# Performance work log

Hardware: AMD Instinct MI355X
Metric: run time of the kernel (lower is better)

## Reference

```python
import jax, jax.numpy as jnp
import numpy as np

N, E, S, K, NB = 16384, 262144, 10, 64, 8
R_MAX, P_CUT, AVG_NEIGH = 5.0, 5, 16.0
L_OF_LM = np.array([0, 1, 1, 1, 2, 2, 2, 2, 2])  # l value of each of the 9 lm components
L_SLICES = [(0, 1), (1, 4), (4, 9)]               # lm ranges for l = 0,1,2
MLP_H = 16


def _sph(u):
    # real spherical harmonics up to l=2, e3nn 'component' normalization (sum_m Y_lm^2 = 2l+1)
    x, y, z = u[..., 0], u[..., 1], u[..., 2]
    s3, s15, s5 = np.float32(np.sqrt(3.0)), np.float32(np.sqrt(15.0)), np.float32(np.sqrt(5.0))
    return jnp.stack([
        jnp.ones_like(x),
        s3 * x, s3 * y, s3 * z,
        s15 * x * y, s15 * y * z, (s5 / 2) * (3 * z * z - 1), s15 * x * z, (s15 / 2) * (x * x - y * y),
    ], axis=-1)


def _radial(r):
    # Bessel radial basis with smooth polynomial cutoff envelope (p = P_CUT)
    u = r / R_MAX
    r_safe = jnp.where(r > 1e-9, r, 1.0)
    n = jnp.arange(1, NB + 1, dtype=r.dtype)
    bess = np.float32(np.sqrt(2.0 / R_MAX)) * jnp.sin(n * jnp.pi * u[:, None]) / r_safe[:, None]
    p = float(P_CUT)
    env = 1.0 - (p + 1) * (p + 2) / 2 * u**P_CUT + p * (p + 2) * u**(P_CUT + 1) - p * (p + 1) / 2 * u**(P_CUT + 2)
    env = jnp.where(u < 1.0, env, 0.0)
    return bess * env[:, None]  # [E, NB]


def setup_inputs() -> dict:
    key = jax.random.key(0)
    ks = jax.random.split(key, 16)
    positions = jax.random.uniform(ks[0], (N, 3), jnp.float32) * 4.0  # box so many edges fall inside r_max
    species = jax.random.randint(ks[1], (N,), 0, S)
    senders = jax.random.randint(ks[2], (E,), 0, N)
    receivers = jax.random.randint(ks[3], (E,), 0, N)
    shifts = jnp.zeros((E, 3), jnp.float32)
    W_embed = jax.random.normal(ks[4], (S, K), jnp.float32)
    W_rad = jax.random.normal(ks[5], (2, 3, NB, K), jnp.float32) * 0.3
    W_mix = jax.random.normal(ks[6], (2, 3, K, K), jnp.float32) / np.sqrt(K)
    W_prod = jax.random.normal(ks[7], (2, 3, 3, K), jnp.float32) * 0.1
    W_sc = jax.random.normal(ks[8], (2, S, 3, K, K), jnp.float32) / np.sqrt(K)
    W_ro0 = jax.random.normal(ks[9], (K,), jnp.float32) / np.sqrt(K)
    W_m1 = jax.random.normal(ks[10], (K, MLP_H), jnp.float32) / np.sqrt(K)
    b_m1 = jnp.zeros((MLP_H,), jnp.float32)
    W_m2 = jax.random.normal(ks[11], (MLP_H,), jnp.float32) / np.sqrt(MLP_H)
    return dict(positions=positions, shifts=shifts, species=species, senders=senders,
                receivers=receivers, W_embed=W_embed, W_rad=W_rad, W_mix=W_mix,
                W_prod=W_prod, W_sc=W_sc, W_ro0=W_ro0, W_m1=W_m1, b_m1=b_m1, W_m2=W_m2)


def reference(positions, shifts, species, senders, receivers, W_embed, W_rad, W_mix,
              W_prod, W_sc, W_ro0, W_m1, b_m1, W_m2):
    lm = jnp.asarray(L_OF_LM)
    onehot = jax.nn.one_hot(species, S, dtype=positions.dtype)
    # node embedding: scalars only -> feats [N, 9(lm), K]
    feats = jnp.zeros((N, 9, K), positions.dtype).at[:, 0, :].set(onehot @ W_embed)

    # edge geometry
    vec = positions[receivers] - positions[senders] + shifts           # [E, 3]
    r = jnp.linalg.norm(vec, axis=-1)                                  # [E]
    u_hat = vec / jnp.where(r > 1e-9, r, 1.0)[:, None]
    Y = _sph(u_hat)                                                     # [E, 9]
    rad = _radial(r)                                                    # [E, NB]

    energies = []
    for i in range(2):
        # interaction: radial-weighted SH messages from sender scalars, scatter-sum to receivers
        hs = feats[:, 0, :][senders]                                    # [E, K]
        Rl = jnp.einsum('eb,lbk->elk', rad, W_rad[i])[:, lm, :]         # [E, 9, K]
        msg = hs[:, None, :] * Y[:, :, None] * Rl                       # [E, 9, K]
        A = jax.ops.segment_sum(msg, receivers, num_segments=N) / AVG_NEIGH
        A = jnp.einsum('nmk,mkj->nmj', A, W_mix[i][lm])                 # per-l channel mixing

        # correlation-3 equivariant product basis (symmetric-contraction style)
        A0 = A[:, 0, :]
        inv = jnp.sum(A * A, axis=1)                                    # rotation-invariant [N, K]
        w1, w2, w3 = (W_prod[i, j][lm] for j in range(3))               # each [9, K]
        B = A * (w1[None] + w2[None] * A0[:, None, :] + w3[None] * inv[:, None, :])

        # species-dependent self-connection (linear of feats x node_attrs), per-l weights
        sc = jnp.concatenate([
            jnp.einsum('nmk,ns,skj->nmj', feats[:, st:en], onehot, W_sc[i, :, l])
            for l, (st, en) in enumerate(L_SLICES)], axis=1)
        feats = B + sc

        if i == 0:
            energies.append(feats[:, 0, :] @ W_ro0)                     # linear readout
        else:
            feats = feats.at[:, 1:, :].set(0.0)                         # last layer keeps 0e only
            energies.append(jax.nn.silu(feats[:, 0, :] @ W_m1 + b_m1) @ W_m2)

    return jnp.stack(energies, axis=1)  # [N, num_interactions]
```

## Files before the change

kernel.cpp:

```cpp
#include <hip/hip_runtime.h>

#define NN 16384
#define NE 262144
#define NSPEC 10
#define KC 64
#define MLPH 16
#define SEG 128
#define EPSG 2048

typedef float v2f __attribute__((ext_vector_type(2)));

__device__ __forceinline__ float wave_reduce(float v) {
#pragma unroll
    for (int off = 32; off > 0; off >>= 1) v += __shfl_down(v, off, 64);
    return v;
}

__device__ __forceinline__ float f4c(const float4& v, int j) {
    const float* p = &v.x;
    return p[j];
}

__global__ void __launch_bounds__(1024) k_pre(
    const float* __restrict__ W_embed,
    const int* __restrict__ species,
    const int* __restrict__ receivers,
    int* __restrict__ eslot,
    unsigned short* __restrict__ cnt16,
    float4* __restrict__ h04) {
    __shared__ int cntL[NN];
    int t = threadIdx.x;
#pragma unroll
    for (int i = 0; i < 16; ++i) cntL[t + 1024 * i] = 0;
    __syncthreads();
    int ebase = blockIdx.x * EPSG;
#pragma unroll
    for (int j = 0; j < EPSG / 1024; ++j) {
        int e = ebase + j * 1024 + t;
        int r = receivers[e];
        eslot[e] = atomicAdd(&cntL[r], 1);
    }
    int gt = blockIdx.x * 1024 + t;
#pragma unroll
    for (int q = 0; q < 2; ++q) {
        int idx = gt * 2 + q;
        int n = idx >> 4, w = idx & 15;
        h04[idx] = reinterpret_cast<const float4*>(W_embed + species[n] * KC)[w];
    }
    __syncthreads();
    unsigned short* o = cnt16 + (size_t)blockIdx.x * NN;
#pragma unroll
    for (int i = 0; i < 16; ++i)
        o[t + 1024 * i] = (unsigned short)cntL[t + 1024 * i];
}

__global__ void __launch_bounds__(256) k_colscan(
    const unsigned short* __restrict__ cnt16,
    int* __restrict__ seg_base,
    int* __restrict__ count) {
    int lane = threadIdx.x & 63;
    int r = blockIdx.x * 4 + (threadIdx.x >> 6);
    int c0 = cnt16[(size_t)(2 * lane) * NN + r];
    int c1 = cnt16[(size_t)(2 * lane + 1) * NN + r];
    int s = c0 + c1;
    int inc = s;
#pragma unroll
    for (int off = 1; off < 64; off <<= 1) {
        int v = __shfl_up(inc, off, 64);
        if (lane >= off) inc += v;
    }
    int exc = inc - s;
    seg_base[(size_t)(2 * lane) * NN + r] = exc;
    seg_base[(size_t)(2 * lane + 1) * NN + r] = exc + c0;
    if (lane == 63) count[r] = inc;
}

__global__ void __launch_bounds__(1024) k_scan(
    const int* __restrict__ count, int* __restrict__ row_start,
    const int* __restrict__ species, int* __restrict__ nslot,
    int* __restrict__ sp_start) {
    __shared__ int lds[1024];
    __shared__ int itercnt[256 * NSPEC];
    __shared__ int spt[NSPEC];
    int t = threadIdx.x;
    int lane = t & 63;
    int w = t >> 6;
#pragma unroll
    for (int j = 0; j < 16; ++j) {
        int n = w * 1024 + j * 64 + lane;
        int sp = species[n];
#pragma unroll
        for (int s = 0; s < NSPEC; ++s) {
            unsigned long long mask = __ballot(sp == s);
            if (lane == 0) itercnt[(w * 16 + j) * NSPEC + s] = (int)__popcll(mask);
        }
    }
    int base = t * 16;
    int local[16];
    int ssum = 0;
#pragma unroll
    for (int b = 0; b < 16; ++b) { local[b] = count[base + b]; ssum += local[b]; }
    lds[t] = ssum;
    __syncthreads();
    for (int off = 1; off < 1024; off <<= 1) {
        int v = (t >= off) ? lds[t - off] : 0;
        __syncthreads();
        lds[t] += v;
        __syncthreads();
    }
    int run = lds[t] - ssum;
#pragma unroll
    for (int b = 0; b < 16; ++b) { row_start[base + b] = run; run += local[b]; }
    if (t == 1023) row_start[NN] = run;
    __syncthreads();
    if (w < NSPEC) {
        int s = w;
        int v0 = itercnt[(lane * 4 + 0) * NSPEC + s];
        int v1 = itercnt[(lane * 4 + 1) * NSPEC + s];
        int v2 = itercnt[(lane * 4 + 2) * NSPEC + s];
        int v3 = itercnt[(lane * 4 + 3) * NSPEC + s];
        int ls = v0 + v1 + v2 + v3;
        int inc = ls;
#pragma unroll
        for (int off = 1; off < 64; off <<= 1) {
            int v = __shfl_up(inc, off, 64);
            if (lane >= off) inc += v;
        }
        int exc = inc - ls;
        itercnt[(lane * 4 + 0) * NSPEC + s] = exc;
        itercnt[(lane * 4 + 1) * NSPEC + s] = exc + v0;
        itercnt[(lane * 4 + 2) * NSPEC + s] = exc + v0 + v1;
        itercnt[(lane * 4 + 3) * NSPEC + s] = exc + v0 + v1 + v2;
        if (lane == 63) spt[s] = inc;
    }
    __syncthreads();
    if (t == 0) {
        int r2 = 0;
        for (int s = 0; s < NSPEC; ++s) { sp_start[s] = r2; r2 += spt[s]; }
        sp_start[NSPEC] = r2;
    }
    __syncthreads();
#pragma unroll
    for (int j = 0; j < 16; ++j) {
        int n = w * 1024 + j * 64 + lane;
        int sp = species[n];
        int rank = 0;
#pragma unroll
        for (int s = 0; s < NSPEC; ++s) {
            unsigned long long mask = __ballot(sp == s);
            if (sp == s)
                rank = (int)__popcll(mask & ((1ull << lane) - 1ull));
        }
        nslot[n] = itercnt[(w * 16 + j) * NSPEC + sp] + rank;
    }
}

__global__ void k_geom(const float* __restrict__ pos,
                       const float* __restrict__ shifts,
                       const int* __restrict__ senders,
                       const int* __restrict__ receivers,
                       const int* __restrict__ row_start,
                       const int* __restrict__ seg_base,
                       const int* __restrict__ eslot,
                       const int* __restrict__ species,
                       const int* __restrict__ sp_start,
                       const int* __restrict__ nslot,
                       int* __restrict__ ord,
                       float* __restrict__ edgerec,
                       int* __restrict__ ssend) {
    int e = blockIdx.x * 256 + threadIdx.x;
    if (e < NN) {
        int sp = species[e];
        ord[sp_start[sp] + nslot[e]] = e;
    }
    int s = senders[e], r = receivers[e];
    float dx = pos[r * 3 + 0] - pos[s * 3 + 0] + shifts[e * 3 + 0];
    float dy = pos[r * 3 + 1] - pos[s * 3 + 1] + shifts[e * 3 + 1];
    float dz = pos[r * 3 + 2] - pos[s * 3 + 2] + shifts[e * 3 + 2];
    float rn = sqrtf(dx * dx + dy * dy + dz * dz);
    float den = (rn > 1e-9f) ? rn : 1.0f;
    float x = dx / den, y = dy / den, z = dz / den;
    const float s3  = 1.7320508075688772f;
    const float s15 = 3.8729833462074170f;
    const float s5h = 1.1180339887498949f;
    const float s15h = 1.9364916731037085f;
    float rec[16];
    rec[0] = s3 * x;
    rec[1] = s3 * y;
    rec[2] = s3 * z;
    rec[3] = s15 * x * y;
    rec[4] = s15 * y * z;
    rec[5] = s5h * (3.0f * z * z - 1.0f);
    rec[6] = s15 * x * z;
    rec[7] = s15h * (x * x - y * y);
    float u = rn * 0.2f;
    float env = 0.0f;
    if (u < 1.0f) {
        float u2 = u * u;
        float u5 = u2 * u2 * u;
        env = 1.0f - 21.0f * u5 + 35.0f * u5 * u - 15.0f * u5 * u2;
    }
    float pre = 0.63245553203367587f * env / den;
    float half_u = 0.5f * u;
#pragma unroll
    for (int nb = 1; nb <= 8; ++nb) {
        float tr = (float)nb * half_u;
        tr -= floorf(tr);
        rec[7 + nb] = pre * __builtin_amdgcn_sinf(tr);
    }
    int p = row_start[r] + seg_base[(size_t)(e >> 11) * NN + r] + eslot[e];
    float4* o = (float4*)(edgerec + (size_t)p * 16);
#pragma unroll
    for (int i = 0; i < 4; ++i)
        o[i] = make_float4(rec[4 * i], rec[4 * i + 1], rec[4 * i + 2], rec[4 * i + 3]);
    ssend[p] = s;
}

#define AMX_NPW 2
__global__ void __launch_bounds__(512, 6) k_aggmix(
    const float* __restrict__ h,
    const float* __restrict__ edgerec,
    const int* __restrict__ ssend,
    const int* __restrict__ row_start,
    const float* __restrict__ Wr_i,
    const float* __restrict__ Wm_i,
    const float* __restrict__ Wp_i,
    float* __restrict__ Bm0) {
    __shared__ float Wlds[2 * 4096];
    __shared__ float xtile[8][9 * 64];
    {
        float4* Wl4 = (float4*)Wlds;
        const float4* W4 = (const float4*)(Wm_i + 4096);
#pragma unroll
        for (int i = 0; i < 4; ++i)
            Wl4[threadIdx.x + 512 * i] = W4[threadIdx.x + 512 * i];
    }
    __syncthreads();
    int lane = threadIdx.x & 63;
    int wid = __builtin_amdgcn_readfirstlane(threadIdx.x >> 6);
    float* xt = xtile[wid];
    float Wr0[8];
    v2f  Wr12[8];
#pragma unroll
    for (int b = 0; b < 8; ++b) {
        Wr0[b]    = Wr_i[b * 64 + lane] * (1.0f / 16.0f);
        Wr12[b].x = Wr_i[(8 + b) * 64 + lane] * (1.0f / 16.0f);
        Wr12[b].y = Wr_i[(16 + b) * 64 + lane] * (1.0f / 16.0f);
    }
    float w10 = Wp_i[0 * 64 + lane];
    float w20 = Wp_i[3 * 64 + lane];
    float w30 = Wp_i[6 * 64 + lane];
    const float* W0g = Wm_i;
    int n0 = (blockIdx.x * 8 + wid) * AMX_NPW;
    for (int it = 0; it < AMX_NPW; ++it) {
        int n = n0 + it;
        float acc0 = 0.f;
        v2f accp[4];
#pragma unroll
        for (int q = 0; q < 4; ++q) accp[q] = (v2f){0.f, 0.f};
        int e0 = row_start[n], e1 = row_start[n + 1];
#pragma unroll 4
        for (int e = e0; e < e1; ++e) {
            int s = ssend[e];
            float hv = h[(size_t)s * 64 + lane];
            const float* rc = edgerec + (size_t)e * 16;
            float R0 = 0.f;
            v2f R12 = (v2f){0.f, 0.f};
#pragma unroll
            for (int b = 0; b < 8; ++b) {
                float rb = rc[8 + b];
                R0 = fmaf(rb, Wr0[b], R0);
                R12 = __builtin_elementwise_fma((v2f){rb, rb}, Wr12[b], R12);
            }
            acc0 = fmaf(hv, R0, acc0);
            float t1 = hv * R12.x, t2 = hv * R12.y;
            accp[0] = __builtin_elementwise_fma((v2f){t1, t1}, (v2f){rc[0], rc[1]}, accp[0]);
            accp[1] = __builtin_elementwise_fma((v2f){t1, t2}, (v2f){rc[2], rc[3]}, accp[1]);
            accp[2] = __builtin_elementwise_fma((v2f){t2, t2}, (v2f){rc[4], rc[5]}, accp[2]);
            accp[3] = __builtin_elementwise_fma((v2f){t2, t2}, (v2f){rc[6], rc[7]}, accp[3]);
        }
        xt[0 * 64 + lane] = acc0;
        xt[1 * 64 + lane] = accp[0].x;  xt[2 * 64 + lane] = accp[0].y;
        xt[3 * 64 + lane] = accp[1].x;  xt[4 * 64 + lane] = accp[1].y;
        xt[5 * 64 + lane] = accp[2].x;  xt[6 * 64 + lane] = accp[2].y;
        xt[7 * 64 + lane] = accp[3].x;  xt[8 * 64 + lane] = accp[3].y;
        v2f mixp[9];
#pragma unroll
        for (int m = 0; m < 9; ++m) mixp[m] = (v2f){0.f, 0.f};
#pragma unroll 2
        for (int c4 = 0; c4 < 16; ++c4) {
            float4 xb[9];
#pragma unroll
            for (int m = 0; m < 9; ++m)
                xb[m] = *(const float4*)&xt[m * 64 + c4 * 4];
#pragma unroll
            for (int j2 = 0; j2 < 2; ++j2) {
                int k0 = c4 * 4 + j2 * 2;
                v2f wv0 = (v2f){W0g[k0 * 64 + lane], W0g[(k0 + 1) * 64 + lane]};
                v2f wv1 = (v2f){Wlds[k0 * 64 + lane], Wlds[(k0 + 1) * 64 + lane]};
                v2f wv2 = (v2f){Wlds[4096 + k0 * 64 + lane], Wlds[4096 + (k0 + 1) * 64 + lane]};
#pragma unroll
                for (int m = 0; m < 9; ++m) {
                    v2f xp = (v2f){f4c(xb[m], j2 * 2), f4c(xb[m], j2 * 2 + 1)};
                    v2f wv = (m == 0) ? wv0 : ((m < 4) ? wv1 : wv2);
                    mixp[m] = __builtin_elementwise_fma(xp, wv, mixp[m]);
                }
            }
        }
        float mix[9];
#pragma unroll
        for (int m = 0; m < 9; ++m) mix[m] = mixp[m].x + mixp[m].y;
        float A0 = mix[0];
        float inv = 0.f;
#pragma unroll
        for (int m = 0; m < 9; ++m) inv += mix[m] * mix[m];
        Bm0[(size_t)n * 64 + lane] = mix[0] * (w10 + w20 * A0 + w30 * inv);
    }
}

#define RPB 32
template <int ITER>
__global__ void __launch_bounds__(256) k_sc(
    const float* __restrict__ h_in,
    const float* __restrict__ Bm0,
    float* __restrict__ h_out,
    const int* __restrict__ ord,
    const int* __restrict__ sp_start,
    const float* __restrict__ Wsc_i,
    const float* __restrict__ W_ro0,
    const float* __restrict__ W_m1,
    const float* __restrict__ b_m1,
    const float* __restrict__ W_m2,
    float* __restrict__ out) {
    const int BPS = NN / RPB;
    int sp = blockIdx.x / BPS;
    int c  = blockIdx.x - sp * BPS;
    int base = sp_start[sp];
    int cnt  = sp_start[sp + 1] - base;
    int r0 = c * RPB;
    __shared__ float Wlds[4096];
    __shared__ float xtile[4][8 * 64];
    if (r0 < cnt) {
        const float4* W4 = (const float4*)(Wsc_i + (size_t)sp * 3 * 4096);
        float4* Wl4 = (float4*)Wlds;
#pragma unroll
        for (int i = 0; i < 4; ++i)
            Wl4[threadIdx.x + 256 * i] = W4[threadIdx.x + 256 * i];
    }
    __syncthreads();
    if (r0 >= cnt) return;
    int lane = threadIdx.x & 63;
    int wid = threadIdx.x >> 6;
    float* xt = xtile[wid];
    int rend = min(r0 + RPB, cnt);
    int q0 = r0 + wid * 8;
    if (q0 >= rend) return;
    int nd[8];
#pragma unroll
    for (int t = 0; t < 8; ++t)
        nd[t] = ord[base + min(q0 + t, rend - 1)];
    float xv[8];
#pragma unroll
    for (int t = 0; t < 8; ++t) xv[t] = h_in[(size_t)nd[t] * 64 + lane];
#pragma unroll
    for (int t = 0; t < 8; ++t) xt[t * 64 + lane] = xv[t];
    float acc[8];
#pragma unroll
    for (int t = 0; t < 8; ++t) acc[t] = 0.f;
#pragma unroll 2
    for (int c4 = 0; c4 < 16; ++c4) {
        float wv[4];
#pragma unroll
        for (int j = 0; j < 4; ++j) wv[j] = Wlds[(c4 * 4 + j) * 64 + lane];
#pragma unroll
        for (int t = 0; t < 8; ++t) {
            float4 xb = *(const float4*)&xt[t * 64 + c4 * 4];
#pragma unroll
            for (int j = 0; j < 4; ++j) acc[t] += f4c(xb, j) * wv[j];
        }
    }
    float wro = W_ro0[lane];
#pragma unroll
    for (int t = 0; t < 8; ++t) {
        if (q0 + t >= rend) break;
        int node = nd[t];
        float outv = acc[t] + Bm0[(size_t)node * 64 + lane];
        if (ITER == 0) {
            h_out[(size_t)node * 64 + lane] = outv;
            float e = wave_reduce(outv * wro);
            if (lane == 0) out[2 * node + 0] = e;
        } else {
            int hh = lane & 15;
            float tacc = b_m1[hh];
#pragma unroll
            for (int k = 0; k < 64; ++k)
                tacc += __shfl(outv, k, 64) * W_m1[k * MLPH + hh];
            float sig = 1.0f / (1.0f + expf(-tacc));
            float contrib = (lane < MLPH) ? tacc * sig * W_m2[lane] : 0.f;
            float e = wave_reduce(contrib);
            if (lane == 0) out[2 * node + 1] = e;
        }
    }
}

extern "C" void kernel_launch(void* const* d_in, const int* in_sizes, int n_in,
                              void* d_out, int out_size, void* d_ws, size_t ws_size,
                              hipStream_t stream) {
    const float* positions = (const float*)d_in[0];
    const float* shifts    = (const float*)d_in[1];
    const int*   species   = (const int*)d_in[2];
    const int*   senders   = (const int*)d_in[3];
    const int*   receivers = (const int*)d_in[4];
    const float* W_embed   = (const float*)d_in[5];
    const float* W_rad     = (const float*)d_in[6];
    const float* W_mix     = (const float*)d_in[7];
    const float* W_prod    = (const float*)d_in[8];
    const float* W_sc      = (const float*)d_in[9];
    const float* W_ro0     = (const float*)d_in[10];
    const float* W_m1      = (const float*)d_in[11];
    const float* b_m1      = (const float*)d_in[12];
    const float* W_m2      = (const float*)d_in[13];
    float* out = (float*)d_out;

    char* p = (char*)d_ws;
    float* edgerec = (float*)p; p += (size_t)NE * 16 * 4;
    int* seg_base  = (int*)p;   p += (size_t)SEG * NN * 4;
    float* Bm0     = (float*)p; p += (size_t)NN * KC * 4;
    float* h0      = (float*)p; p += (size_t)NN * KC * 4;
    float* h1      = (float*)p; p += (size_t)NN * KC * 4;
    unsigned short* cnt16 = (unsigned short*)p; p += (size_t)SEG * NN * 2;
    int* eslot     = (int*)p; p += (size_t)NE * 4;
    int* ssend     = (int*)p; p += (size_t)NE * 4;
    int* nslot     = (int*)p; p += (size_t)NN * 4;
    int* ord       = (int*)p; p += (size_t)NN * 4;
    int* count     = (int*)p; p += (size_t)NN * 4;
    int* row_start = (int*)p; p += (size_t)(NN + 1) * 4;
    int* sp_start  = (int*)p; p += 16 * 4;

    k_pre<<<SEG, 1024, 0, stream>>>(W_embed, species, receivers,
                                    eslot, cnt16, (float4*)h0);
    k_colscan<<<NN / 4, 256, 0, stream>>>(cnt16, seg_base, count);
    k_scan<<<1, 1024, 0, stream>>>(count, row_start, species, nslot, sp_start);
    k_geom<<<NE / 256, 256, 0, stream>>>(positions, shifts, senders, receivers,
                                         row_start, seg_base, eslot, species,
                                         sp_start, nslot, ord, edgerec, ssend);

    k_aggmix<<<NN / (8 * AMX_NPW), 512, 0, stream>>>(h0, edgerec, ssend, row_start,
        W_rad + 0, W_mix + 0, W_prod + 0, Bm0);
    k_sc<0><<<NSPEC * (NN / RPB), 256, 0, stream>>>(h0, Bm0, h1, ord, sp_start,
        W_sc + 0, W_ro0, W_m1, b_m1, W_m2, out);

    k_aggmix<<<NN / (8 * AMX_NPW), 512, 0, stream>>>(h1, edgerec, ssend, row_start,
        W_rad + 1536, W_mix + 12288, W_prod + 576, Bm0);
    k_sc<1><<<NSPEC * (NN / RPB), 256, 0, stream>>>(h1, Bm0, h0 , ord,
        sp_start, W_sc + (size_t)NSPEC * 3 * 4096, W_ro0, W_m1, b_m1, W_m2, out);
}
```

Before: 295.2 us.

## Interleave two nodes' edge loops in aggmix; simplify column scan; shrink sc grid

The aggregation kernel now walks the edge lists of a wave's two receiver nodes side by side, issuing both nodes' gathers together to get more memory-level parallelism, then runs the two tails separately. The column scan becomes one thread per receiver looping serially over the 128 segments, replacing the wave-wide shuffle scan. The self-connection kernel launches a fixed 160 blocks per species instead of N/32. Far fewer of those blocks exit immediately, but this silently assumes no species has more than 5120 nodes.

Result: faster. 273.4 us (-7.4%).

```diff
diff --git a/kernel.cpp b/kernel.cpp
--- a/kernel.cpp
+++ b/kernel.cpp
@@ -7,6 +7,7 @@
 #define MLPH 16
 #define SEG 128
 #define EPSG 2048
+#define SC_BPS 160
 
 typedef float v2f __attribute__((ext_vector_type(2)));
 
@@ -54,25 +55,19 @@
         o[t + 1024 * i] = (unsigned short)cntL[t + 1024 * i];
 }
 
-__global__ void __launch_bounds__(256) k_colscan(
+__global__ void __launch_bounds__(128) k_colscan(
     const unsigned short* __restrict__ cnt16,
     int* __restrict__ seg_base,
     int* __restrict__ count) {
-    int lane = threadIdx.x & 63;
-    int r = blockIdx.x * 4 + (threadIdx.x >> 6);
-    int c0 = cnt16[(size_t)(2 * lane) * NN + r];
-    int c1 = cnt16[(size_t)(2 * lane + 1) * NN + r];
-    int s = c0 + c1;
-    int inc = s;
-#pragma unroll
-    for (int off = 1; off < 64; off <<= 1) {
-        int v = __shfl_up(inc, off, 64);
-        if (lane >= off) inc += v;
-    }
-    int exc = inc - s;
-    seg_base[(size_t)(2 * lane) * NN + r] = exc;
-    seg_base[(size_t)(2 * lane + 1) * NN + r] = exc + c0;
-    if (lane == 63) count[r] = inc;
+    int r = blockIdx.x * 128 + threadIdx.x;
+    int run = 0;
+#pragma unroll 4
+    for (int g = 0; g < SEG; ++g) {
+        int c = cnt16[(size_t)g * NN + r];
+        seg_base[(size_t)g * NN + r] = run;
+        run += c;
+    }
+    count[r] = run;
 }
 
 __global__ void __launch_bounds__(1024) k_scan(
@@ -216,7 +211,26 @@
     ssend[p] = s;
 }
 
-#define AMX_NPW 2
+__device__ __forceinline__ void agg_edge_pk(
+    const float* __restrict__ rc, float hv,
+    const float (&Wr0)[8], const v2f (&Wr12)[8],
+    float& acc0, v2f (&accp)[4]) {
+    float R0 = 0.f;
+    v2f R12 = (v2f){0.f, 0.f};
+#pragma unroll
+    for (int b = 0; b < 8; ++b) {
+        float rb = rc[8 + b];
+        R0 = fmaf(rb, Wr0[b], R0);
+        R12 = __builtin_elementwise_fma((v2f){rb, rb}, Wr12[b], R12);
+    }
+    acc0 = fmaf(hv, R0, acc0);
+    float t1 = hv * R12.x, t2 = hv * R12.y;
+    accp[0] = __builtin_elementwise_fma((v2f){t1, t1}, (v2f){rc[0], rc[1]}, accp[0]);
+    accp[1] = __builtin_elementwise_fma((v2f){t1, t2}, (v2f){rc[2], rc[3]}, accp[1]);
+    accp[2] = __builtin_elementwise_fma((v2f){t2, t2}, (v2f){rc[4], rc[5]}, accp[2]);
+    accp[3] = __builtin_elementwise_fma((v2f){t2, t2}, (v2f){rc[6], rc[7]}, accp[3]);
+}
+
 __global__ void __launch_bounds__(512, 6) k_aggmix(
     const float* __restrict__ h,
     const float* __restrict__ edgerec,
@@ -251,39 +265,55 @@
     float w20 = Wp_i[3 * 64 + lane];
     float w30 = Wp_i[6 * 64 + lane];
     const float* W0g = Wm_i;
-    int n0 = (blockIdx.x * 8 + wid) * AMX_NPW;
-    for (int it = 0; it < AMX_NPW; ++it) {
-        int n = n0 + it;
-        float acc0 = 0.f;
-        v2f accp[4];
-#pragma unroll
-        for (int q = 0; q < 4; ++q) accp[q] = (v2f){0.f, 0.f};
-        int e0 = row_start[n], e1 = row_start[n + 1];
-#pragma unroll 4
-        for (int e = e0; e < e1; ++e) {
-            int s = ssend[e];
-            float hv = h[(size_t)s * 64 + lane];
-            const float* rc = edgerec + (size_t)e * 16;
-            float R0 = 0.f;
-            v2f R12 = (v2f){0.f, 0.f};
-#pragma unroll
-            for (int b = 0; b < 8; ++b) {
-                float rb = rc[8 + b];
-                R0 = fmaf(rb, Wr0[b], R0);
-                R12 = __builtin_elementwise_fma((v2f){rb, rb}, Wr12[b], R12);
-            }
-            acc0 = fmaf(hv, R0, acc0);
-            float t1 = hv * R12.x, t2 = hv * R12.y;
-            accp[0] = __builtin_elementwise_fma((v2f){t1, t1}, (v2f){rc[0], rc[1]}, accp[0]);
-            accp[1] = __builtin_elementwise_fma((v2f){t1, t2}, (v2f){rc[2], rc[3]}, accp[1]);
-            accp[2] = __builtin_elementwise_fma((v2f){t2, t2}, (v2f){rc[4], rc[5]}, accp[2]);
-            accp[3] = __builtin_elementwise_fma((v2f){t2, t2}, (v2f){rc[6], rc[7]}, accp[3]);
-        }
-        xt[0 * 64 + lane] = acc0;
-        xt[1 * 64 + lane] = accp[0].x;  xt[2 * 64 + lane] = accp[0].y;
-        xt[3 * 64 + lane] = accp[1].x;  xt[4 * 64 + lane] = accp[1].y;
-        xt[5 * 64 + lane] = accp[2].x;  xt[6 * 64 + lane] = accp[2].y;
-        xt[7 * 64 + lane] = accp[3].x;  xt[8 * 64 + lane] = accp[3].y;
+
+    int nA = (blockIdx.x * 8 + wid) * 2;
+    int nB = nA + 1;
+    int eA0 = row_start[nA], eA1 = row_start[nA + 1], eB1 = row_start[nB + 1];
+    int eB0 = eA1;
+    int cA = eA1 - eA0, cB = eB1 - eB0;
+    int mc = min(cA, cB);
+
+    float accA0 = 0.f, accB0 = 0.f;
+    v2f accAp[4], accBp[4];
+#pragma unroll
+    for (int q = 0; q < 4; ++q) { accAp[q] = (v2f){0.f, 0.f}; accBp[q] = (v2f){0.f, 0.f}; }
+
+#pragma unroll 2
+    for (int i = 0; i < mc; ++i) {
+        int ea = eA0 + i, eb = eB0 + i;
+        int sa = ssend[ea], sb = ssend[eb];
+        float ha = h[(size_t)sa * 64 + lane];
+        float hb = h[(size_t)sb * 64 + lane];
+        const float* ra = edgerec + (size_t)ea * 16;
+        const float* rb = edgerec + (size_t)eb * 16;
+        agg_edge_pk(ra, ha, Wr0, Wr12, accA0, accAp);
+        agg_edge_pk(rb, hb, Wr0, Wr12, accB0, accBp);
+    }
+#pragma unroll 2
+    for (int i = mc; i < cA; ++i) {
+        int ea = eA0 + i;
+        int sa = ssend[ea];
+        float ha = h[(size_t)sa * 64 + lane];
+        agg_edge_pk(edgerec + (size_t)ea * 16, ha, Wr0, Wr12, accA0, accAp);
+    }
+#pragma unroll 2
+    for (int i = mc; i < cB; ++i) {
+        int eb = eB0 + i;
+        int sb = ssend[eb];
+        float hb = h[(size_t)sb * 64 + lane];
+        agg_edge_pk(edgerec + (size_t)eb * 16, hb, Wr0, Wr12, accB0, accBp);
+    }
+
+#pragma unroll
+    for (int nn = 0; nn < 2; ++nn) {
+        float a0 = nn ? accB0 : accA0;
+        v2f* ap = nn ? accBp : accAp;
+        int n = nn ? nB : nA;
+        xt[0 * 64 + lane] = a0;
+        xt[1 * 64 + lane] = ap[0].x;  xt[2 * 64 + lane] = ap[0].y;
+        xt[3 * 64 + lane] = ap[1].x;  xt[4 * 64 + lane] = ap[1].y;
+        xt[5 * 64 + lane] = ap[2].x;  xt[6 * 64 + lane] = ap[2].y;
+        xt[7 * 64 + lane] = ap[3].x;  xt[8 * 64 + lane] = ap[3].y;
         v2f mixp[9];
 #pragma unroll
         for (int m = 0; m < 9; ++m) mixp[m] = (v2f){0.f, 0.f};
@@ -332,9 +362,8 @@
     const float* __restrict__ b_m1,
     const float* __restrict__ W_m2,
     float* __restrict__ out) {
-    const int BPS = NN / RPB;
-    int sp = blockIdx.x / BPS;
-    int c  = blockIdx.x - sp * BPS;
+    int sp = blockIdx.x / SC_BPS;
+    int c  = blockIdx.x - sp * SC_BPS;
     int base = sp_start[sp];
     int cnt  = sp_start[sp + 1] - base;
     int r0 = c * RPB;
@@ -439,19 +468,19 @@
 
     k_pre<<<SEG, 1024, 0, stream>>>(W_embed, species, receivers,
                                     eslot, cnt16, (float4*)h0);
-    k_colscan<<<NN / 4, 256, 0, stream>>>(cnt16, seg_base, count);
+    k_colscan<<<NN / 128, 128, 0, stream>>>(cnt16, seg_base, count);
     k_scan<<<1, 1024, 0, stream>>>(count, row_start, species, nslot, sp_start);
     k_geom<<<NE / 256, 256, 0, stream>>>(positions, shifts, senders, receivers,
                                          row_start, seg_base, eslot, species,
                                          sp_start, nslot, ord, edgerec, ssend);
 
-    k_aggmix<<<NN / (8 * AMX_NPW), 512, 0, stream>>>(h0, edgerec, ssend, row_start,
+    k_aggmix<<<NN / 16, 512, 0, stream>>>(h0, edgerec, ssend, row_start,
         W_rad + 0, W_mix + 0, W_prod + 0, Bm0);
-    k_sc<0><<<NSPEC * (NN / RPB), 256, 0, stream>>>(h0, Bm0, h1, ord, sp_start,
+    k_sc<0><<<NSPEC * SC_BPS, 256, 0, stream>>>(h0, Bm0, h1, ord, sp_start,
         W_sc + 0, W_ro0, W_m1, b_m1, W_m2, out);
 
-    k_aggmix<<<NN / (8 * AMX_NPW), 512, 0, stream>>>(h1, edgerec, ssend, row_start,
+    k_aggmix<<<NN / 16, 512, 0, stream>>>(h1, edgerec, ssend, row_start,
         W_rad + 1536, W_mix + 12288, W_prod + 576, Bm0);
-    k_sc<1><<<NSPEC * (NN / RPB), 256, 0, stream>>>(h1, Bm0, h0 , ord,
+    k_sc<1><<<NSPEC * SC_BPS, 256, 0, stream>>>(h1, Bm0, h0 , ord,
         sp_start, W_sc + (size_t)NSPEC * 3 * 4096, W_ro0, W_m1, b_m1, W_m2, out);
 }
```
